# Optimization experiments

Hardware: AMD Instinct MI355X
Metric: run time of the kernel (lower is better)

Reference implementation:

```python
import jax, jax.numpy as jnp
import numpy as np

L, N, K, S, V, H = 12, 2048, 8, 4, 50000, 256


def setup_inputs() -> dict:
    key = jax.random.key(0)
    ks = jax.random.split(key, 20)
    tokens1 = jax.random.randint(ks[0], (L, N, S), 0, V, dtype=jnp.int32)
    tokens2 = jax.random.randint(ks[1], (L, N, S), 0, V, dtype=jnp.int32)
    # child indices into previous level's h (0 = zero-init row, -1 = no child)
    idx1 = jax.random.randint(ks[2], (L, N, K), -1, N + 1, dtype=jnp.int32).at[0].set(-1)
    idx2 = jax.random.randint(ks[3], (L, N, K), -1, N + 1, dtype=jnp.int32).at[0].set(-1)
    sc = 0.02
    E = jax.random.normal(ks[4], (V, H), jnp.float32)  # torch.randn init
    lin_W = jax.random.normal(ks[5], (H * S, H), jnp.float32) * sc
    lin_b = jnp.zeros((H,), jnp.float32)
    Uf_W = jax.random.normal(ks[6], (H, H), jnp.float32) * sc
    Uf_b = jnp.zeros((H,), jnp.float32)
    Uiuo_W = jax.random.normal(ks[7], (H, 3 * H), jnp.float32) * sc
    Uiuo_b = jnp.zeros((3 * H,), jnp.float32)
    W_W = jax.random.normal(ks[8], (H, 4 * H), jnp.float32) * sc
    W_b = jnp.zeros((4 * H,), jnp.float32)
    dense_W = jax.random.normal(ks[9], (H, 512), jnp.float32) * sc
    dense_b = jnp.zeros((512,), jnp.float32)
    out_W = jax.random.normal(ks[10], (512, 2), jnp.float32) * sc
    out_b = jnp.zeros((2,), jnp.float32)
    return dict(tokens1=tokens1, idx1=idx1, tokens2=tokens2, idx2=idx2,
                E=E, lin_W=lin_W, lin_b=lin_b, Uf_W=Uf_W, Uf_b=Uf_b,
                Uiuo_W=Uiuo_W, Uiuo_b=Uiuo_b, W_W=W_W, W_b=W_b,
                dense_W=dense_W, dense_b=dense_b, out_W=out_W, out_b=out_b)


def _encode(tokens, idx, E, lin_W, lin_b, Uf_W, Uf_b, Uiuo_W, Uiuo_b, W_W, W_b):
    # TreeEmbeddingLayer: lookup label_size tokens per node, concat, linear
    emb = E[tokens].reshape(L, N, S * H)           # [L,N,S*H]
    x = emb @ lin_W + lin_b                        # [L,N,H]

    def step(carry, inp):
        h_prev, c_prev = carry                     # [N,H]
        xl, il = inp                               # [N,H], [N,K]
        zero = jnp.zeros((1, H), xl.dtype)
        hp = jnp.concatenate([zero, h_prev], 0)    # [N+1,H] (row 0 = init)
        cp = jnp.concatenate([zero, c_prev], 0)
        mask_bool = il != -1
        index = jnp.where(mask_bool, il, 0)
        h = hp[index]                              # [N,K,H] gather child states
        c = cp[index]
        m = mask_bool[..., None].astype(xl.dtype)  # [N,K,1]
        h_sum = jnp.sum(h * m, axis=1)             # [N,H]
        Wx = xl @ W_W + W_b                        # [N,4H]
        Wf, Wi, Wu, Wo = Wx[:, :H], Wx[:, H:2*H], Wx[:, 2*H:3*H], Wx[:, 3*H:]
        fk = jax.nn.sigmoid(Wf[:, None, :] + h @ Uf_W + Uf_b)  # [N,K,H]
        bf = jnp.sum(fk * c * m, axis=1)           # [N,H]
        iuo = h_sum @ Uiuo_W + Uiuo_b              # [N,3H]
        i = jax.nn.sigmoid(iuo[:, :H] + Wi)
        u = jnp.tanh(iuo[:, H:2*H] + Wu)
        o = jax.nn.sigmoid(iuo[:, 2*H:] + Wo)
        nc = i * u + bf
        nh = o * jnp.tanh(nc)
        return (nh, nc), nh

    init = (jnp.zeros((N, H), x.dtype), jnp.zeros((N, H), x.dtype))
    (_, _), hs = jax.lax.scan(step, init, (x, idx))
    # 1 layer with skip connection; hx = last (root) level
    return hs[-1] + x[-1]                          # [N,H]


def reference(tokens1, idx1, tokens2, idx2, E, lin_W, lin_b, Uf_W, Uf_b,
              Uiuo_W, Uiuo_b, W_W, W_b, dense_W, dense_b, out_W, out_b):
    h1 = _encode(tokens1, idx1, E, lin_W, lin_b, Uf_W, Uf_b, Uiuo_W, Uiuo_b, W_W, W_b)
    h2 = _encode(tokens2, idx2, E, lin_W, lin_b, Uf_W, Uf_b, Uiuo_W, Uiuo_b, W_W, W_b)
    abs_dist = jnp.abs(h1 - h2)                    # [N,H]
    x = jnp.tanh(abs_dist @ dense_W + dense_b)     # dropout = identity (eval)
    logits = x @ out_W + out_b                     # [N,2]
    return jax.nn.softmax(logits, axis=-1)
```

## Files before the change

kernel.cpp:

```cpp
#include <hip/hip_runtime.h>

#define LL 12
#define NN 2048
#define KK 8
#define SS 4
#define HH 256
#define LN (LL*NN)
#define VV 50000
#define ZROW 4096
#define SROW 2048

typedef __bf16 bf16_t;
typedef __bf16 bf16x8 __attribute__((ext_vector_type(8)));
typedef __bf16 bf16x4v __attribute__((ext_vector_type(4)));
typedef float f32x4 __attribute__((ext_vector_type(4)));

__device__ __forceinline__ float sigmoidf_(float x) { return 1.f / (1.f + expf(-x)); }

__global__ __launch_bounds__(256) void k_cvtE(const float* __restrict__ src,
                                              bf16_t* __restrict__ dst, int n4)
{
    int i = blockIdx.x * 256 + threadIdx.x;
    const int stride = gridDim.x * 256;
    for (; i < n4; i += stride) {
        const float4 v = ((const float4*)src)[i];
        bf16x4v o;
        o[0] = (bf16_t)v.x; o[1] = (bf16_t)v.y; o[2] = (bf16_t)v.z; o[3] = (bf16_t)v.w;
        ((bf16x4v*)dst)[i] = o;
    }
}

__global__ __launch_bounds__(256) void k_cvtW(
    const float* __restrict__ linW, const float* __restrict__ WW,
    const float* __restrict__ UfW, const float* __restrict__ UiW,
    bf16_t* __restrict__ linWt, bf16_t* __restrict__ WWt,
    bf16_t* __restrict__ UfWt, bf16_t* __restrict__ UiWt)
{
    int i = blockIdx.x * 256 + threadIdx.x;
    if (i < 262144) {
        const int rr = i >> 8, cc = i & 255;
        linWt[(size_t)cc * 1024 + rr] = (bf16_t)linW[i];
        return;
    }
    i -= 262144;
    if (i < 262144) {
        const int rr = i >> 10, cc = i & 1023;
        WWt[(size_t)cc * 256 + rr] = (bf16_t)WW[i];
        return;
    }
    i -= 262144;
    if (i < 65536) {
        const int rr = i >> 8, cc = i & 255;
        UfWt[(size_t)cc * 256 + rr] = (bf16_t)UfW[i];
        return;
    }
    i -= 65536;
    if (i < 196608) {
        const int rr = i / 768, cc = i - rr * 768;
        UiWt[(size_t)cc * 256 + rr] = (bf16_t)UiW[i];
    }
}

__global__ __launch_bounds__(256) void k_zero(float* __restrict__ SA, float* __restrict__ SB)
{
    const int t = threadIdx.x;
    float* a = SA + (size_t)ZROW * 512;
    float* b = SB + (size_t)ZROW * 512;
    a[t] = 0.f; a[t + 256] = 0.f;
    b[t] = 0.f; b[t + 256] = 0.f;
}

__global__ __launch_bounds__(256) void k_embed(
    const int* __restrict__ tok1, const int* __restrict__ tok2,
    const bf16_t* __restrict__ Ebf, const bf16_t* __restrict__ linWt,
    const float* __restrict__ linb, bf16_t* __restrict__ xout)
{
    __shared__ int toff[64][SS];
    const int t = threadIdx.x;
    const int m0 = blockIdx.x * 64;
    {
        const int lr = t >> 2, s = t & 3;
        const int m = m0 + lr;
        const int e = (m >= LN) ? 1 : 0;
        const int rrow = m - e * LN;
        const int* tok = e ? tok2 : tok1;
        toff[lr][s] = tok[(size_t)rrow * SS + s] * HH;
    }
    __syncthreads();
    const int lane = t & 63, w = t >> 6;
    const int wm = w >> 1, wn = w & 1;
    const int r = lane & 15, kg = lane >> 4;
    const int lr0 = wm * 32 + r, lr1 = lr0 + 16;
    const bf16_t* bp[8];
    #pragma unroll
    for (int j = 0; j < 8; ++j)
        bp[j] = linWt + (size_t)(wn * 128 + j * 16 + r) * 1024 + kg * 8;

    const f32x4 zero = {0.f, 0.f, 0.f, 0.f};
    f32x4 acc[2][8];
    #pragma unroll
    for (int mi = 0; mi < 2; ++mi)
        #pragma unroll
        for (int j = 0; j < 8; ++j) acc[mi][j] = zero;

    for (int k0 = 0; k0 < 1024; k0 += 32) {
        const int s = k0 >> 8, off = (k0 & 255) + kg * 8;
        const bf16x8 a0 = *(const bf16x8*)(Ebf + (size_t)toff[lr0][s] + off);
        const bf16x8 a1 = *(const bf16x8*)(Ebf + (size_t)toff[lr1][s] + off);
        #pragma unroll
        for (int j = 0; j < 8; ++j) {
            const bf16x8 b = *(const bf16x8*)bp[j];
            acc[0][j] = __builtin_amdgcn_mfma_f32_16x16x32_bf16(a0, b, acc[0][j], 0, 0, 0);
            acc[1][j] = __builtin_amdgcn_mfma_f32_16x16x32_bf16(a1, b, acc[1][j], 0, 0, 0);
            bp[j] += 32;
        }
    }
    const int crow = m0 + wm * 32 + kg * 4;
    #pragma unroll
    for (int j = 0; j < 8; ++j) {
        const int ccol = wn * 128 + j * 16 + r;
        const float bv = linb[ccol];
        #pragma unroll
        for (int mi = 0; mi < 2; ++mi)
            #pragma unroll
            for (int jj = 0; jj < 4; ++jj)
                xout[(size_t)(crow + mi * 16 + jj) * HH + ccol] =
                    (bf16_t)(acc[mi][j][jj] + bv);
    }
}

__global__ __launch_bounds__(512, 2) void k_step(
    const bf16_t* __restrict__ xbf,
    const int* __restrict__ idx1, const int* __restrict__ idx2, const int l,
    const bf16_t* __restrict__ UfWt, const float* __restrict__ Ufb,
    const bf16_t* __restrict__ UiWt, const float* __restrict__ Uib,
    const bf16_t* __restrict__ WWt, const float* __restrict__ Wb,
    const char* __restrict__ Sprev, char* __restrict__ Snext)
{
    __shared__ __align__(16) bf16_t WxL[16 * 1024];
    __shared__ __align__(16) bf16_t iuoL[16 * 768];
    __shared__ __align__(16) bf16_t hsumL[16 * 256];

    const int t = threadIdx.x;
    const int bid = blockIdx.x;
    const int x  = bid & 7;
    const int e  = x >> 2;
    const int n0 = ((bid >> 3) * 4 + (x & 3)) * 16;
    const int g0 = e * NN + n0;
    const int lane = t & 63, w = t >> 6;
    const int r = lane & 15, kg = lane >> 4;
    const f32x4 zero = {0.f, 0.f, 0.f, 0.f};

    const int rr = t >> 5, sl = t & 31;
    const int ss = (sl + 4 * (rr & 7)) & 31;

    int ch[KK];
    {
        const int* idxp = (e ? idx2 : idx1) + ((size_t)l * NN + n0 + rr) * KK;
        const int4 i0 = *(const int4*)idxp;
        const int4 i1 = *(const int4*)(idxp + 4);
        ch[0] = i0.x; ch[1] = i0.y; ch[2] = i0.z; ch[3] = i0.w;
        ch[4] = i1.x; ch[5] = i1.y; ch[6] = i1.z; ch[7] = i1.w;
        #pragma unroll
        for (int k = 0; k < KK; ++k)
            ch[k] = (ch[k] >= 1) ? (e * NN + ch[k] - 1) : ZROW;
    }

    bf16x8 hv[KK];
    #pragma unroll
    for (int k = 0; k < KK; ++k)
        hv[k] = *(const bf16x8*)(Sprev + (size_t)ch[k] * SROW + 1024 + sl * 16);

    const bf16_t* xrow = xbf + ((size_t)e * LN + (size_t)l * NN + n0 + r) * HH + kg * 8;
    bf16x8 aWx[8];
    #pragma unroll
    for (int k = 0; k < 8; ++k) aWx[k] = *(const bf16x8*)(xrow + k * 32);

    {
        const bf16_t* bw[8];
        #pragma unroll
        for (int j = 0; j < 8; ++j)
            bw[j] = WWt + (size_t)((8 * w + j) * 16 + r) * HH + kg * 8;
        f32x4 acc[8];
        #pragma unroll
        for (int j = 0; j < 8; ++j) acc[j] = zero;
        #pragma unroll
        for (int k = 0; k < 8; ++k) {
            #pragma unroll
            for (int j = 0; j < 8; ++j) {
                const bf16x8 b = *(const bf16x8*)bw[j];
                acc[j] = __builtin_amdgcn_mfma_f32_16x16x32_bf16(aWx[k], b, acc[j], 0, 0, 0);
                bw[j] += 32;
            }
        }
        #pragma unroll
        for (int j = 0; j < 8; ++j) {
            const int col = (8 * w + j) * 16 + r;
            const float bv = Wb[col];
            #pragma unroll
            for (int jj = 0; jj < 4; ++jj)
                WxL[(size_t)(kg * 4 + jj) * 1024 + col] = (bf16_t)(acc[j][jj] + bv);
        }
    }

    {
        float hs[8] = {0.f, 0.f, 0.f, 0.f, 0.f, 0.f, 0.f, 0.f};
        #pragma unroll
        for (int k = 0; k < KK; ++k) {
            #pragma unroll
            for (int j = 0; j < 8; ++j) hs[j] += (float)hv[k][j];
        }
        bf16x8 o;
        #pragma unroll
        for (int j = 0; j < 8; ++j) o[j] = (bf16_t)hs[j];
        *(bf16x8*)(hsumL + rr * 256 + ss * 8) = o;
    }
    __syncthreads();

    float4 cv0[KK], cv1[KK];
    bf16x8 fv[KK];
    #pragma unroll
    for (int k = 0; k < KK; ++k) {
        const char* row = Sprev + (size_t)ch[k] * SROW;
        cv0[k] = *(const float4*)(row + sl * 32);
        cv1[k] = *(const float4*)(row + sl * 32 + 16);
        fv[k]  = *(const bf16x8*)(row + 1536 + sl * 16);
    }

    {
        const bf16_t* bu[6];
        #pragma unroll
        for (int j = 0; j < 6; ++j)
            bu[j] = UiWt + (size_t)((6 * w + j) * 16 + r) * HH + kg * 8;
        f32x4 acc[6];
        #pragma unroll
        for (int j = 0; j < 6; ++j) acc[j] = zero;
        for (int k0 = 0; k0 < HH; k0 += 32) {
            const int sa = (((k0 >> 3) + kg) + 4 * (r & 7)) & 31;
            const bf16x8 a = *(const bf16x8*)(hsumL + r * 256 + sa * 8);
            #pragma unroll
            for (int j = 0; j < 6; ++j) {
                const bf16x8 b = *(const bf16x8*)bu[j];
                acc[j] = __builtin_amdgcn_mfma_f32_16x16x32_bf16(a, b, acc[j], 0, 0, 0);
                bu[j] += 32;
            }
        }
        #pragma unroll
        for (int j = 0; j < 6; ++j) {
            const int col = (6 * w + j) * 16 + r;
            const float bv = Uib[col];
            #pragma unroll
            for (int jj = 0; jj < 4; ++jj)
                iuoL[(size_t)(kg * 4 + jj) * 768 + col] = (bf16_t)(acc[j][jj] + bv);
        }
    }

    float ba[8] = {0.f, 0.f, 0.f, 0.f, 0.f, 0.f, 0.f, 0.f};
    {
        float wf[8];
        const bf16x8 wv = *(const bf16x8*)(WxL + (size_t)rr * 1024 + sl * 8);
        #pragma unroll
        for (int j = 0; j < 8; ++j) wf[j] = (float)wv[j];
        #pragma unroll
        for (int k = 0; k < KK; ++k) {
            const float cc[8] = {cv0[k].x, cv0[k].y, cv0[k].z, cv0[k].w,
                                 cv1[k].x, cv1[k].y, cv1[k].z, cv1[k].w};
            #pragma unroll
            for (int j = 0; j < 8; ++j) {
                const float fk = sigmoidf_(wf[j] + (float)fv[k][j]);
                ba[j] = fmaf(fk, cc[j], ba[j]);
            }
        }
    }
    __syncthreads();

    {
        const bf16x8 wiv = *(const bf16x8*)(WxL + (size_t)rr * 1024 + 256 + sl * 8);
        const bf16x8 wuv = *(const bf16x8*)(WxL + (size_t)rr * 1024 + 512 + sl * 8);
        const bf16x8 wov = *(const bf16x8*)(WxL + (size_t)rr * 1024 + 768 + sl * 8);
        const bf16x8 iv  = *(const bf16x8*)(iuoL + (size_t)rr * 768 + sl * 8);
        const bf16x8 uv  = *(const bf16x8*)(iuoL + (size_t)rr * 768 + 256 + sl * 8);
        const bf16x8 ov  = *(const bf16x8*)(iuoL + (size_t)rr * 768 + 512 + sl * 8);
        float nc[8];
        bf16x8 nhb;
        #pragma unroll
        for (int j = 0; j < 8; ++j) {
            const float ig = sigmoidf_((float)iv[j] + (float)wiv[j]);
            const float ug = tanhf((float)uv[j] + (float)wuv[j]);
            const float og = sigmoidf_((float)ov[j] + (float)wov[j]);
            nc[j] = fmaf(ig, ug, ba[j]);
            nhb[j] = (bf16_t)(og * tanhf(nc[j]));
        }
        char* rowN = Snext + (size_t)(g0 + rr) * SROW;
        const f32x4 c0 = {nc[0], nc[1], nc[2], nc[3]};
        const f32x4 c1 = {nc[4], nc[5], nc[6], nc[7]};
        *(f32x4*)(rowN + sl * 32) = c0;
        *(f32x4*)(rowN + sl * 32 + 16) = c1;
        *(bf16x8*)(rowN + 1024 + sl * 16) = nhb;
        *(bf16x8*)(hsumL + rr * 256 + ss * 8) = nhb;
    }

    if (l < LL - 1) {
        __syncthreads();
        const int ct0 = 2 * w;
        const bf16_t* bq0 = UfWt + (size_t)(ct0 * 16 + r) * HH + kg * 8;
        const bf16_t* bq1 = bq0 + (size_t)16 * HH;
        f32x4 ac0 = zero, ac1 = zero;
        for (int k0 = 0; k0 < HH; k0 += 32) {
            const int sa = (((k0 >> 3) + kg) + 4 * (r & 7)) & 31;
            const bf16x8 a = *(const bf16x8*)(hsumL + r * 256 + sa * 8);
            const bf16x8 b0 = *(const bf16x8*)bq0;
            const bf16x8 b1 = *(const bf16x8*)bq1;
            ac0 = __builtin_amdgcn_mfma_f32_16x16x32_bf16(a, b0, ac0, 0, 0, 0);
            ac1 = __builtin_amdgcn_mfma_f32_16x16x32_bf16(a, b1, ac1, 0, 0, 0);
            bq0 += 32; bq1 += 32;
        }
        const int c0 = ct0 * 16 + r, c1 = c0 + 16;
        const float bv0 = Ufb[c0], bv1 = Ufb[c1];
        #pragma unroll
        for (int jj = 0; jj < 4; ++jj) {
            bf16_t* fr = (bf16_t*)(Snext + (size_t)(g0 + kg * 4 + jj) * SROW + 1536);
            fr[c0] = (bf16_t)(ac0[jj] + bv0);
            fr[c1] = (bf16_t)(ac1[jj] + bv1);
        }
    }
}

__global__ __launch_bounds__(256) void k_final(
    const char* __restrict__ Sfin, const bf16_t* __restrict__ xbf,
    const float* __restrict__ dW, const float* __restrict__ db,
    const float* __restrict__ oW, const float* __restrict__ ob,
    float* __restrict__ out)
{
    __shared__ __align__(16) float ad[8][HH];
    __shared__ __align__(16) float xx[8][512];
    const int t = threadIdx.x;
    const int n0 = blockIdx.x * 8;
    const size_t xoff1 = (size_t)(LL - 1) * NN * HH;
    const size_t xoff2 = (size_t)LN * HH + xoff1;
    #pragma unroll
    for (int rr = 0; rr < 8; ++rr) {
        const int n = n0 + rr;
        const float h1 = (float)((const bf16_t*)(Sfin + (size_t)n * SROW + 1024))[t]
                       + (float)xbf[xoff1 + (size_t)n * HH + t];
        const float h2 = (float)((const bf16_t*)(Sfin + (size_t)(NN + n) * SROW + 1024))[t]
                       + (float)xbf[xoff2 + (size_t)n * HH + t];
        ad[rr][t] = fabsf(h1 - h2);
    }
    __syncthreads();
    float a0[8], a1[8];
    #pragma unroll
    for (int rr = 0; rr < 8; ++rr) { a0[rr] = 0.f; a1[rr] = 0.f; }
    for (int k = 0; k < HH; k += 4) {
        #pragma unroll
        for (int kk = 0; kk < 4; ++kk) {
            const float b0 = dW[(size_t)(k + kk) * 512 + t];
            const float b1 = dW[(size_t)(k + kk) * 512 + 256 + t];
            #pragma unroll
            for (int rr = 0; rr < 8; ++rr) {
                const float av = ad[rr][k + kk];
                a0[rr] = fmaf(av, b0, a0[rr]);
                a1[rr] = fmaf(av, b1, a1[rr]);
            }
        }
    }
    const float db0 = db[t], db1 = db[256 + t];
    #pragma unroll
    for (int rr = 0; rr < 8; ++rr) {
        xx[rr][t] = tanhf(a0[rr] + db0);
        xx[rr][256 + t] = tanhf(a1[rr] + db1);
    }
    __syncthreads();
    const int w = t >> 6, lane = t & 63;
    for (int rr = w; rr < 8; rr += 4) {
        float p0 = 0.f, p1 = 0.f;
        for (int k = lane; k < 512; k += 64) {
            const float xv = xx[rr][k];
            p0 = fmaf(xv, oW[2 * k + 0], p0);
            p1 = fmaf(xv, oW[2 * k + 1], p1);
        }
        #pragma unroll
        for (int off = 32; off > 0; off >>= 1) {
            p0 += __shfl_down(p0, off);
            p1 += __shfl_down(p1, off);
        }
        if (lane == 0) {
            const float l0 = p0 + ob[0], l1 = p1 + ob[1];
            const float mx = fmaxf(l0, l1);
            const float e0 = expf(l0 - mx), e1 = expf(l1 - mx);
            const float inv = 1.f / (e0 + e1);
            out[(size_t)(n0 + rr) * 2 + 0] = e0 * inv;
            out[(size_t)(n0 + rr) * 2 + 1] = e1 * inv;
        }
    }
}

extern "C" void kernel_launch(void* const* d_in, const int* in_sizes, int n_in,
                              void* d_out, int out_size, void* d_ws, size_t ws_size,
                              hipStream_t stream) {
    (void)in_sizes; (void)n_in; (void)out_size; (void)ws_size;
    const int*   tok1 = (const int*)d_in[0];
    const int*   idx1 = (const int*)d_in[1];
    const int*   tok2 = (const int*)d_in[2];
    const int*   idx2 = (const int*)d_in[3];
    const float* E    = (const float*)d_in[4];
    const float* linW = (const float*)d_in[5];
    const float* linb = (const float*)d_in[6];
    const float* UfW  = (const float*)d_in[7];
    const float* Ufb  = (const float*)d_in[8];
    const float* UiW  = (const float*)d_in[9];
    const float* Uib  = (const float*)d_in[10];
    const float* WW   = (const float*)d_in[11];
    const float* Wb   = (const float*)d_in[12];
    const float* dW   = (const float*)d_in[13];
    const float* db   = (const float*)d_in[14];
    const float* oW   = (const float*)d_in[15];
    const float* ob   = (const float*)d_in[16];
    float* out = (float*)d_out;

    bf16_t* xbf = (bf16_t*)d_ws;
    char*   uni = (char*)(xbf + (size_t)12582912);
    bf16_t* Ebf = (bf16_t*)uni;
    char*   SA  = uni;
    char*   SB  = uni + 8390656;
    bf16_t* linWt = (bf16_t*)(uni + 25600000);
    bf16_t* WWt   = linWt + (size_t)262144;
    bf16_t* UfWt  = WWt   + (size_t)262144;
    bf16_t* UiWt  = UfWt  + (size_t)65536;

    k_cvtE<<<2048, 256, 0, stream>>>(E, Ebf, VV * HH / 4);
    k_cvtW<<<3072, 256, 0, stream>>>(linW, WW, UfW, UiW, linWt, WWt, UfWt, UiWt);

    k_embed<<<768, 256, 0, stream>>>(tok1, tok2, Ebf, linWt, linb, xbf);

    k_zero<<<1, 256, 0, stream>>>((float*)SA, (float*)SB);

    char *Sp = SA, *Sn = SB;
    for (int l = 0; l < LL; ++l) {
        k_step<<<256, 512, 0, stream>>>(xbf, idx1, idx2, l,
                                        UfWt, Ufb, UiWt, Uib, WWt, Wb, Sp, Sn);
        char* ts = Sp; Sp = Sn; Sn = ts;
    }

    k_final<<<NN / 8, 256, 0, stream>>>(Sp, xbf, dW, db, oW, ob, out);
}
```

Measured before the change: 707.0 us.

## Precompute per-slot vocab projection table and gather-sum embeddings

Reassociates the embedding linear layer: instead of gathering token embeddings and running a 1024-wide GEMM per node, it projects the whole vocabulary through each slot's slice of lin_W into a bf16 table G. Each node's input then becomes a sum of four gathered rows. This removes the separate E-to-bf16 conversion pass and the per-node GEMM. In exchange it does a vocabulary-sized GEMM whose FLOP count is close to the one it replaces, writes a roughly 100MB table, and adds an extra bf16 rounding before the sum. The new path only runs when the workspace is large enough; otherwise the old path is kept.

```diff
diff --git a/kernel.cpp b/kernel.cpp
--- a/kernel.cpp
+++ b/kernel.cpp
@@ -68,6 +68,91 @@
     float* b = SB + (size_t)ZROW * 512;
     a[t] = 0.f; a[t + 256] = 0.f;
     b[t] = 0.f; b[t + 256] = 0.f;
+}
+
+__global__ __launch_bounds__(256) void k_G(
+    const float* __restrict__ E, const bf16_t* __restrict__ linWt,
+    const float* __restrict__ linb, bf16_t* __restrict__ G)
+{
+    const int s = blockIdx.x;
+    const int m0 = blockIdx.y * 64;
+    const int t = threadIdx.x;
+    const int lane = t & 63, w = t >> 6;
+    const int wm = w >> 1, wn = w & 1;
+    const int r = lane & 15, kg = lane >> 4;
+    const int row0 = m0 + wm * 32 + r, row1 = row0 + 16;
+    const float* a0p = E + (size_t)(row0 < VV ? row0 : 0) * HH + kg * 8;
+    const float* a1p = E + (size_t)(row1 < VV ? row1 : 0) * HH + kg * 8;
+    const bf16_t* bp[8];
+    #pragma unroll
+    for (int j = 0; j < 8; ++j)
+        bp[j] = linWt + (size_t)(wn * 128 + j * 16 + r) * 1024 + s * 256 + kg * 8;
+
+    const f32x4 zero = {0.f, 0.f, 0.f, 0.f};
+    f32x4 acc[2][8];
+    #pragma unroll
+    for (int mi = 0; mi < 2; ++mi)
+        #pragma unroll
+        for (int j = 0; j < 8; ++j) acc[mi][j] = zero;
+
+    for (int k0 = 0; k0 < 256; k0 += 32) {
+        const float4 u0 = *(const float4*)(a0p + k0);
+        const float4 u1 = *(const float4*)(a0p + k0 + 4);
+        const float4 v0 = *(const float4*)(a1p + k0);
+        const float4 v1 = *(const float4*)(a1p + k0 + 4);
+        bf16x8 a0, a1;
+        a0[0] = (bf16_t)u0.x; a0[1] = (bf16_t)u0.y; a0[2] = (bf16_t)u0.z; a0[3] = (bf16_t)u0.w;
+        a0[4] = (bf16_t)u1.x; a0[5] = (bf16_t)u1.y; a0[6] = (bf16_t)u1.z; a0[7] = (bf16_t)u1.w;
+        a1[0] = (bf16_t)v0.x; a1[1] = (bf16_t)v0.y; a1[2] = (bf16_t)v0.z; a1[3] = (bf16_t)v0.w;
+        a1[4] = (bf16_t)v1.x; a1[5] = (bf16_t)v1.y; a1[6] = (bf16_t)v1.z; a1[7] = (bf16_t)v1.w;
+        #pragma unroll
+        for (int j = 0; j < 8; ++j) {
+            const bf16x8 b = *(const bf16x8*)bp[j];
+            acc[0][j] = __builtin_amdgcn_mfma_f32_16x16x32_bf16(a0, b, acc[0][j], 0, 0, 0);
+            acc[1][j] = __builtin_amdgcn_mfma_f32_16x16x32_bf16(a1, b, acc[1][j], 0, 0, 0);
+            bp[j] += 32;
+        }
+    }
+    const int crow = m0 + wm * 32 + kg * 4;
+    bf16_t* Gs = G + (size_t)s * VV * HH;
+    #pragma unroll
+    for (int j = 0; j < 8; ++j) {
+        const int ccol = wn * 128 + j * 16 + r;
+        const float bv = (s == 0) ? linb[ccol] : 0.f;
+        #pragma unroll
+        for (int mi = 0; mi < 2; ++mi)
+            #pragma unroll
+            for (int jj = 0; jj < 4; ++jj) {
+                const int grow = crow + mi * 16 + jj;
+                if (grow < VV)
+                    Gs[(size_t)grow * HH + ccol] = (bf16_t)(acc[mi][j][jj] + bv);
+            }
+    }
+}
+
+__global__ __launch_bounds__(256) void k_embed2(
+    const int* __restrict__ tok1, const int* __restrict__ tok2,
+    const bf16_t* __restrict__ G, bf16_t* __restrict__ xbf)
+{
+    const int t = threadIdx.x;
+    const int m0 = blockIdx.x * 64;
+    const int sl = t & 31, rb = t >> 5;
+    #pragma unroll
+    for (int i = 0; i < 8; ++i) {
+        const int m = m0 + rb + i * 8;
+        const int e = (m >= LN) ? 1 : 0;
+        const int rrow = m - e * LN;
+        const int4 tk = *(const int4*)((e ? tok2 : tok1) + (size_t)rrow * SS);
+        const bf16x8 g0 = *(const bf16x8*)(G + ((size_t)0 * VV + tk.x) * HH + sl * 8);
+        const bf16x8 g1 = *(const bf16x8*)(G + ((size_t)1 * VV + tk.y) * HH + sl * 8);
+        const bf16x8 g2 = *(const bf16x8*)(G + ((size_t)2 * VV + tk.z) * HH + sl * 8);
+        const bf16x8 g3 = *(const bf16x8*)(G + ((size_t)3 * VV + tk.w) * HH + sl * 8);
+        bf16x8 o;
+        #pragma unroll
+        for (int j = 0; j < 8; ++j)
+            o[j] = (bf16_t)((float)g0[j] + (float)g1[j] + (float)g2[j] + (float)g3[j]);
+        *(bf16x8*)(xbf + (size_t)m * HH + sl * 8) = o;
+    }
 }
 
 __global__ __launch_bounds__(256) void k_embed(
@@ -398,7 +483,7 @@
 extern "C" void kernel_launch(void* const* d_in, const int* in_sizes, int n_in,
                               void* d_out, int out_size, void* d_ws, size_t ws_size,
                               hipStream_t stream) {
-    (void)in_sizes; (void)n_in; (void)out_size; (void)ws_size;
+    (void)in_sizes; (void)n_in; (void)out_size;
     const int*   tok1 = (const int*)d_in[0];
     const int*   idx1 = (const int*)d_in[1];
     const int*   tok2 = (const int*)d_in[2];
@@ -418,29 +503,52 @@
     const float* ob   = (const float*)d_in[16];
     float* out = (float*)d_out;
 
+    const size_t NEED_G = 25165824ull + 102400000ull + 1572864ull;
     bf16_t* xbf = (bf16_t*)d_ws;
     char*   uni = (char*)(xbf + (size_t)12582912);
-    bf16_t* Ebf = (bf16_t*)uni;
-    char*   SA  = uni;
-    char*   SB  = uni + 8390656;
-    bf16_t* linWt = (bf16_t*)(uni + 25600000);
-    bf16_t* WWt   = linWt + (size_t)262144;
-    bf16_t* UfWt  = WWt   + (size_t)262144;
-    bf16_t* UiWt  = UfWt  + (size_t)65536;
-
-    k_cvtE<<<2048, 256, 0, stream>>>(E, Ebf, VV * HH / 4);
-    k_cvtW<<<3072, 256, 0, stream>>>(linW, WW, UfW, UiW, linWt, WWt, UfWt, UiWt);
-
-    k_embed<<<768, 256, 0, stream>>>(tok1, tok2, Ebf, linWt, linb, xbf);
-
-    k_zero<<<1, 256, 0, stream>>>((float*)SA, (float*)SB);
-
-    char *Sp = SA, *Sn = SB;
-    for (int l = 0; l < LL; ++l) {
-        k_step<<<256, 512, 0, stream>>>(xbf, idx1, idx2, l,
-                                        UfWt, Ufb, UiWt, Uib, WWt, Wb, Sp, Sn);
-        char* ts = Sp; Sp = Sn; Sn = ts;
-    }
-
-    k_final<<<NN / 8, 256, 0, stream>>>(Sp, xbf, dW, db, oW, ob, out);
-}
+
+    if (ws_size >= NEED_G) {
+        bf16_t* G   = (bf16_t*)uni;
+        char*   SA  = uni;
+        char*   SB  = uni + 8390656;
+        char*   wts = uni + 102400000;
+        bf16_t* linWt = (bf16_t*)wts;
+        bf16_t* WWt   = linWt + (size_t)262144;
+        bf16_t* UfWt  = WWt   + (size_t)262144;
+        bf16_t* UiWt  = UfWt  + (size_t)65536;
+
+        k_cvtW<<<3072, 256, 0, stream>>>(linW, WW, UfW, UiW, linWt, WWt, UfWt, UiWt);
+        k_G<<<dim3(4, (VV + 63) / 64), 256, 0, stream>>>(E, linWt, linb, G);
+        k_embed2<<<768, 256, 0, stream>>>(tok1, tok2, G, xbf);
+        k_zero<<<1, 256, 0, stream>>>((float*)SA, (float*)SB);
+
+        char *Sp = SA, *Sn = SB;
+        for (int l = 0; l < LL; ++l) {
+            k_step<<<256, 512, 0, stream>>>(xbf, idx1, idx2, l,
+                                            UfWt, Ufb, UiWt, Uib, WWt, Wb, Sp, Sn);
+            char* ts = Sp; Sp = Sn; Sn = ts;
+        }
+        k_final<<<NN / 8, 256, 0, stream>>>(Sp, xbf, dW, db, oW, ob, out);
+    } else {
+        bf16_t* Ebf = (bf16_t*)uni;
+        char*   SA  = uni;
+        char*   SB  = uni + 8390656;
+        bf16_t* linWt = (bf16_t*)(uni + 25600000);
+        bf16_t* WWt   = linWt + (size_t)262144;
+        bf16_t* UfWt  = WWt   + (size_t)262144;
+        bf16_t* UiWt  = UfWt  + (size_t)65536;
+
+        k_cvtE<<<2048, 256, 0, stream>>>(E, Ebf, VV * HH / 4);
+        k_cvtW<<<3072, 256, 0, stream>>>(linW, WW, UfW, UiW, linWt, WWt, UfWt, UiWt);
+        k_embed<<<768, 256, 0, stream>>>(tok1, tok2, Ebf, linWt, linb, xbf);
+        k_zero<<<1, 256, 0, stream>>>((float*)SA, (float*)SB);
+
+        char *Sp = SA, *Sn = SB;
+        for (int l = 0; l < LL; ++l) {
+            k_step<<<256, 512, 0, stream>>>(xbf, idx1, idx2, l,
+                                            UfWt, Ufb, UiWt, Uib, WWt, Wb, Sp, Sn);
+            char* ts = Sp; Sp = Sn; Sn = ts;
+        }
+        k_final<<<NN / 8, 256, 0, stream>>>(Sp, xbf, dW, db, oW, ob, out);
+    }
+}
```

Result: slower. 777.2 us (+9.9%).
